# Kernel tuning notes

Measured on AMD Instinct MI355X. Metric: run time of the kernel, lower is better.

The kernel has to match this reference:

```python
import jax, jax.numpy as jnp
import numpy as np

B, P, K, HE, HF = 256, 128, 512, 1024, 512
D = K + HE + 2 * HF  # 2560, MLP input dim
HID = 64


def setup_inputs() -> dict:
    key = jax.random.key(0)
    ks = jax.random.split(key, 6)
    query = jax.random.normal(ks[0], (B, 1, HE), dtype=jnp.float32)
    keys = jax.random.normal(ks[1], (B, P, K), dtype=jnp.float32)
    frameLSTM_h = jax.random.normal(ks[2], (B, 1, 2 * HF), dtype=jnp.float32)
    mask = jax.random.randint(ks[3], (B, P), 0, 2, dtype=jnp.int32)
    mask = mask.at[:, 0].set(1)  # guarantee at least one unmasked player per row
    W1 = jax.random.normal(ks[4], (D, HID), dtype=jnp.float32) / np.float32(np.sqrt(D))
    W2 = jax.random.normal(ks[5], (HID, 1), dtype=jnp.float32) / np.float32(np.sqrt(HID))
    return dict(query=query, keys=keys, frameLSTM_h=frameLSTM_h, mask=mask, W1=W1, W2=W2)


def reference(query, keys, frameLSTM_h, mask, W1, W2):
    # Faithful to: cat([keys, query.repeat, frame.repeat]) @ W1 -> ReLU -> @ W2.
    # The pre-activation is linear, so splitting W1 by row-blocks is exactly the
    # same math without materializing the repeated/concatenated (B,P,D) tensor.
    W1k = W1[:K]            # (K, 64)
    W1q = W1[K:K + HE]      # (HE, 64)
    W1f = W1[K + HE:]       # (2*HF, 64)
    h = jax.nn.relu(
        jnp.einsum('bpk,kh->bph', keys, W1k)
        + jnp.einsum('boe,eh->boh', query, W1q)        # broadcasts over P
        + jnp.einsum('bof,fh->boh', frameLSTM_h, W1f)  # broadcasts over P
    )  # (B, P, 64)
    raw_scores = jnp.einsum('bph,ho->bp', h, W2)  # (B, P)
    raw_scores = jnp.where(mask == 0, -jnp.inf, raw_scores)
    weights = jax.nn.softmax(raw_scores, axis=1)  # (B, P)
    context = jnp.einsum('bp,bpk->bk', weights, keys)[:, None, :]  # (B, 1, K)
    embeddings = jnp.concatenate([context, frameLSTM_h], axis=2)   # (B, 1, K+2*HF)
    return embeddings, weights
```

## Files before the change

### kernel.cpp

```cpp
#include <hip/hip_runtime.h>
#include <hip/hip_bf16.h>
#include <cstdint>
#include <math.h>


typedef __bf16 bf16;
typedef __attribute__((ext_vector_type(8))) __bf16 bf16x8;
typedef __attribute__((ext_vector_type(4))) __bf16 bf16x4;
typedef __attribute__((ext_vector_type(4))) float f32x4;

#define NB 256
#define NP 128
#define NK 512
#define SKLD 520
#define SK_BYTES (NP * SKLD * 2)
#define SMEM_BYTES (SK_BYTES + 128*4 + 128*4 + 256*4 + 64*4)

__global__ __launch_bounds__(256) void prep_kernel(
    const float* __restrict__ W1, bf16* __restrict__ w1kt,
    bf16* __restrict__ w1qft)
{
    const int blk = blockIdx.x;
    const int t = threadIdx.x;
    __shared__ float s[32][65];
    if (blk < 16) {
        const int k0 = blk * 32;
#pragma unroll
        for (int i = 0; i < 8; i++) {
            const int idx = t + 256 * i;
            const int k = idx >> 6, h = idx & 63;
            s[k][h] = W1[(size_t)(k0 + k) * 64 + h];
        }
        __syncthreads();
#pragma unroll
        for (int i = 0; i < 8; i++) {
            const int idx = t + 256 * i;
            const int h = idx >> 5, kk = idx & 31;
            w1kt[(size_t)h * 512 + k0 + kk] = (bf16)s[kk][h];
        }
    } else {
        const int j = blk - 16;
        const int d0 = j * 32;
#pragma unroll
        for (int i = 0; i < 8; i++) {
            const int idx = t + 256 * i;
            const int r = idx >> 6, h = idx & 63;
            s[r][h] = W1[(size_t)(512 + d0 + r) * 64 + h];
        }
        __syncthreads();
#pragma unroll
        for (int i = 0; i < 8; i++) {
            const int idx = t + 256 * i;
            const int h = idx >> 5, rr = idx & 31;
            w1qft[(size_t)h * 2048 + d0 + rr] = (bf16)s[rr][h];
        }
    }
}

__global__ __launch_bounds__(256) void attn_kernel(
    const float* __restrict__ keys, const float* __restrict__ query,
    const float* __restrict__ frame, const int* __restrict__ mask,
    const float* __restrict__ W2, const bf16* __restrict__ w1kt,
    const bf16* __restrict__ w1qft, float* __restrict__ out)
{
    extern __shared__ char smem[];
    bf16* sk      = (bf16*)smem;
    float* scores = (float*)(smem + SK_BYTES);
    float* wts    = scores + 128;
    float* pp     = wts + 128;
    float* w2l    = pp + 256;

    const int b = blockIdx.x;
    const int t = threadIdx.x;
    const int w = t >> 6;
    const int lane = t & 63;
    const int m = lane & 15;
    const int q = lane >> 4;

    if (t < 64) w2l[t] = W2[t];

    {
        const float* qf = (w < 2 ? query : frame) + (size_t)b * 1024 + (w & 1) * 512;
        const bf16* wb = w1qft + (size_t)m * 2048 + w * 512 + q * 8;
        f32x4 pacc[4];
#pragma unroll
        for (int nt = 0; nt < 4; nt++) pacc[nt] = (f32x4){0.f, 0.f, 0.f, 0.f};

        float4 qa = *(const float4*)(qf + q * 8);
        float4 qb = *(const float4*)(qf + q * 8 + 4);
        bf16x8 Bp[4];
#pragma unroll
        for (int nt = 0; nt < 4; nt++) Bp[nt] = *(const bf16x8*)(wb + nt * 32768);

#pragma unroll
        for (int kk = 0; kk < 16; kk++) {
            bf16x8 Af;
            Af[0] = (bf16)qa.x; Af[1] = (bf16)qa.y; Af[2] = (bf16)qa.z; Af[3] = (bf16)qa.w;
            Af[4] = (bf16)qb.x; Af[5] = (bf16)qb.y; Af[6] = (bf16)qb.z; Af[7] = (bf16)qb.w;
            bf16x8 Bc[4];
#pragma unroll
            for (int nt = 0; nt < 4; nt++) Bc[nt] = Bp[nt];
            if (kk < 15) {
                qa = *(const float4*)(qf + (kk + 1) * 32 + q * 8);
                qb = *(const float4*)(qf + (kk + 1) * 32 + q * 8 + 4);
#pragma unroll
                for (int nt = 0; nt < 4; nt++)
                    Bp[nt] = *(const bf16x8*)(wb + nt * 32768 + (kk + 1) * 32);
            }
#pragma unroll
            for (int nt = 0; nt < 4; nt++)
                pacc[nt] = __builtin_amdgcn_mfma_f32_16x16x32_bf16(Af, Bc[nt], pacc[nt], 0, 0, 0);
        }
        if (q == 0) {
#pragma unroll
            for (int nt = 0; nt < 4; nt++)
                pp[w * 64 + nt * 16 + m] = pacc[nt][0];
        }
    }

    const float* kb = keys + (size_t)b * (NP * NK);
    {
        const int rowadd = t >> 7;
        const int c0 = (t & 127) * 4;
        float4 kv[2][16];
#pragma unroll
        for (int ii = 0; ii < 16; ii++)
            kv[0][ii] = *(const float4*)(kb + (size_t)ii * 1024 + t * 4);
#pragma unroll
        for (int jj = 0; jj < 4; jj++) {
            const int cur = jj & 1;
            if (jj < 3) {
#pragma unroll
                for (int ii = 0; ii < 16; ii++)
                    kv[cur ^ 1][ii] =
                        *(const float4*)(kb + (size_t)((jj + 1) * 16 + ii) * 1024 + t * 4);
            }
#pragma unroll
            for (int ii = 0; ii < 16; ii++) {
                const float4 v = kv[cur][ii];
                bf16x4 bv;
                bv[0] = (bf16)v.x; bv[1] = (bf16)v.y;
                bv[2] = (bf16)v.z; bv[3] = (bf16)v.w;
                *(bf16x4*)(sk + (size_t)(2 * (jj * 16 + ii) + rowadd) * SKLD + c0) = bv;
            }
        }
    }
    __syncthreads();

    const int pw = w * 32;
    const bf16* bbase = w1kt + (size_t)m * 512 + q * 8;

    bf16x8 Bv[2][16];
#pragma unroll
    for (int kk = 0; kk < 16; kk++)
        Bv[0][kk] = *(const bf16x8*)(bbase + kk * 32);

    float pr[2][4] = {{0.f,0.f,0.f,0.f},{0.f,0.f,0.f,0.f}};

#pragma unroll
    for (int nt = 0; nt < 4; nt++) {
        const int cur = nt & 1;
        if (nt < 3) {
#pragma unroll
            for (int kk = 0; kk < 16; kk++)
                Bv[cur ^ 1][kk] = *(const bf16x8*)(bbase + (nt + 1) * 8192 + kk * 32);
        }
        f32x4 acc0 = (f32x4){0.f,0.f,0.f,0.f};
        f32x4 acc1 = (f32x4){0.f,0.f,0.f,0.f};
#pragma unroll
        for (int kk = 0; kk < 16; kk++) {
            const int k0 = kk * 32 + q * 8;
            const bf16x8 A0 = *(const bf16x8*)(sk + (pw + m) * SKLD + k0);
            const bf16x8 A1 = *(const bf16x8*)(sk + (pw + 16 + m) * SKLD + k0);
            acc0 = __builtin_amdgcn_mfma_f32_16x16x32_bf16(A0, Bv[cur][kk], acc0, 0, 0, 0);
            acc1 = __builtin_amdgcn_mfma_f32_16x16x32_bf16(A1, Bv[cur][kk], acc1, 0, 0, 0);
        }
        const int h = nt * 16 + m;
        const float pv = pp[h] + pp[64 + h] + pp[128 + h] + pp[192 + h];
        const float wv = w2l[h];
#pragma unroll
        for (int r = 0; r < 4; r++) {
            pr[0][r] += fmaxf(acc0[r] + pv, 0.f) * wv;
            pr[1][r] += fmaxf(acc1[r] + pv, 0.f) * wv;
        }
    }

#pragma unroll
    for (int off = 1; off < 16; off <<= 1) {
#pragma unroll
        for (int mt = 0; mt < 2; mt++)
#pragma unroll
            for (int r = 0; r < 4; r++)
                pr[mt][r] += __shfl_xor(pr[mt][r], off);
    }
    if (m == 0) {
#pragma unroll
        for (int mt = 0; mt < 2; mt++) {
            const int pbase = pw + mt * 16 + q * 4;
#pragma unroll
            for (int r = 0; r < 4; r++) scores[pbase + r] = pr[mt][r];
        }
    }
    __syncthreads();

    if (w == 0) {
        const int pa = lane, pb = lane + 64;
        float s0 = (mask[b * 128 + pa] == 0) ? -INFINITY : scores[pa];
        float s1 = (mask[b * 128 + pb] == 0) ? -INFINITY : scores[pb];
        float mx = fmaxf(s0, s1);
#pragma unroll
        for (int off = 32; off; off >>= 1) mx = fmaxf(mx, __shfl_xor(mx, off));
        float e0 = __expf(s0 - mx), e1 = __expf(s1 - mx);
        float sum = e0 + e1;
#pragma unroll
        for (int off = 32; off; off >>= 1) sum += __shfl_xor(sum, off);
        const float inv = 1.0f / sum;
        e0 *= inv; e1 *= inv;
        wts[pa] = e0; wts[pb] = e1;
        float* wout = out + (size_t)NB * 1536;
        wout[b * 128 + pa] = e0;
        wout[b * 128 + pb] = e1;
    }
    __syncthreads();

    {
        float a0 = 0.f, a1 = 0.f;
        const int c = 2 * t;
#pragma unroll 8
        for (int p = 0; p < 128; p++) {
            const float wv = wts[p];
            const uint32_t uv = *(const uint32_t*)(sk + p * SKLD + c);
            a0 += wv * __uint_as_float(uv << 16);
            a1 += wv * __uint_as_float(uv & 0xffff0000u);
        }
        out[(size_t)b * 1536 + c] = a0;
        out[(size_t)b * 1536 + c + 1] = a1;
    }
    {
        const float4 fv = *(const float4*)(frame + (size_t)b * 1024 + t * 4);
        *(float4*)(out + (size_t)b * 1536 + 512 + t * 4) = fv;
    }
}

extern "C" void kernel_launch(void* const* d_in, const int* in_sizes, int n_in,
                              void* d_out, int out_size, void* d_ws, size_t ws_size,
                              hipStream_t stream) {
    const float* query = (const float*)d_in[0];
    const float* keys  = (const float*)d_in[1];
    const float* frame = (const float*)d_in[2];
    const int*   mask  = (const int*)d_in[3];
    const float* W1    = (const float*)d_in[4];
    const float* W2    = (const float*)d_in[5];
    float* out = (float*)d_out;

    bf16* w1kt  = (bf16*)d_ws;
    bf16* w1qft = (bf16*)((char*)d_ws + (64 << 10));

    hipFuncSetAttribute((const void*)attn_kernel,
                        hipFuncAttributeMaxDynamicSharedMemorySize, SMEM_BYTES);

    prep_kernel<<<80, 256, 0, stream>>>(W1, w1kt, w1qft);
    attn_kernel<<<256, 256, SMEM_BYTES, stream>>>(keys, query, frame, mask, W2,
                                                  w1kt, w1qft, out);
}
```

Baseline: 124.6 us.

## Move query/frame projection to prep kernel and fuse keys load with MFMA

The per-batch query/frame projection moves out of the attention kernel into the prep kernel, which now computes it in fp32 for 4 batches per block. The attention kernel uses 512 threads, and each wave streams its 16 key rows straight from global memory into bf16 MFMA operands while also writing them to shared memory. This removes the separate staging pass and the extra sync before the score GEMM. The context reduction now gives each thread one column. The trade-off is a serial fp32 dot-product loop in the prep kernel that may take longer, and more threads per block.

New measurement: 154.7 us. +24.2%, slower.

```diff
diff --git a/kernel.cpp b/kernel.cpp
--- a/kernel.cpp
+++ b/kernel.cpp
@@ -6,7 +6,6 @@
 
 typedef __bf16 bf16;
 typedef __attribute__((ext_vector_type(8))) __bf16 bf16x8;
-typedef __attribute__((ext_vector_type(4))) __bf16 bf16x4;
 typedef __attribute__((ext_vector_type(4))) float f32x4;
 
 #define NB 256
@@ -14,16 +13,17 @@
 #define NK 512
 #define SKLD 520
 #define SK_BYTES (NP * SKLD * 2)
-#define SMEM_BYTES (SK_BYTES + 128*4 + 128*4 + 256*4 + 64*4)
+#define SMEM_BYTES (SK_BYTES + 128 * 4 + 128 * 4)
 
 __global__ __launch_bounds__(256) void prep_kernel(
-    const float* __restrict__ W1, bf16* __restrict__ w1kt,
-    bf16* __restrict__ w1qft)
+    const float* __restrict__ W1, const float* __restrict__ query,
+    const float* __restrict__ frame, bf16* __restrict__ w1kt,
+    float* __restrict__ proj)
 {
     const int blk = blockIdx.x;
     const int t = threadIdx.x;
-    __shared__ float s[32][65];
     if (blk < 16) {
+        __shared__ float s[32][65];
         const int k0 = blk * 32;
 #pragma unroll
         for (int i = 0; i < 8; i++) {
@@ -39,36 +39,43 @@
             w1kt[(size_t)h * 512 + k0 + kk] = (bf16)s[kk][h];
         }
     } else {
-        const int j = blk - 16;
-        const int d0 = j * 32;
-#pragma unroll
-        for (int i = 0; i < 8; i++) {
-            const int idx = t + 256 * i;
-            const int r = idx >> 6, h = idx & 63;
-            s[r][h] = W1[(size_t)(512 + d0 + r) * 64 + h];
-        }
+        __shared__ float red[4][4][64];
+        const int b0 = (blk - 16) * 4;
+        const int c = t >> 6;
+        const int h = t & 63;
+        const float* q0 = (c < 2) ? (query + c * 512) : (frame + (c - 2) * 512);
+        const float* w1r = W1 + (size_t)(512 + c * 512) * 64 + h;
+        float a0[4] = {0.f, 0.f, 0.f, 0.f};
+        float a1[4] = {0.f, 0.f, 0.f, 0.f};
+#pragma unroll 4
+        for (int d = 0; d < 512; d += 2) {
+            const float w0  = w1r[(size_t)d * 64];
+            const float w1v = w1r[(size_t)(d + 1) * 64];
+#pragma unroll
+            for (int j = 0; j < 4; j++) {
+                a0[j] += q0[(size_t)(b0 + j) * 1024 + d] * w0;
+                a1[j] += q0[(size_t)(b0 + j) * 1024 + d + 1] * w1v;
+            }
+        }
+#pragma unroll
+        for (int j = 0; j < 4; j++) red[c][j][h] = a0[j] + a1[j];
         __syncthreads();
-#pragma unroll
-        for (int i = 0; i < 8; i++) {
-            const int idx = t + 256 * i;
-            const int h = idx >> 5, rr = idx & 31;
-            w1qft[(size_t)h * 2048 + d0 + rr] = (bf16)s[rr][h];
-        }
+        const int j2 = t >> 6;
+        proj[(size_t)(b0 + j2) * 64 + h] =
+            red[0][j2][h] + red[1][j2][h] + red[2][j2][h] + red[3][j2][h];
     }
 }
 
-__global__ __launch_bounds__(256) void attn_kernel(
-    const float* __restrict__ keys, const float* __restrict__ query,
-    const float* __restrict__ frame, const int* __restrict__ mask,
-    const float* __restrict__ W2, const bf16* __restrict__ w1kt,
-    const bf16* __restrict__ w1qft, float* __restrict__ out)
+__global__ __launch_bounds__(512) void attn_kernel(
+    const float* __restrict__ keys, const float* __restrict__ frame,
+    const int* __restrict__ mask, const float* __restrict__ W2,
+    const bf16* __restrict__ w1kt, const float* __restrict__ proj,
+    float* __restrict__ out)
 {
     extern __shared__ char smem[];
     bf16* sk      = (bf16*)smem;
     float* scores = (float*)(smem + SK_BYTES);
     float* wts    = scores + 128;
-    float* pp     = wts + 128;
-    float* w2l    = pp + 256;
 
     const int b = blockIdx.x;
     const int t = threadIdx.x;
@@ -76,135 +83,72 @@
     const int lane = t & 63;
     const int m = lane & 15;
     const int q = lane >> 4;
-
-    if (t < 64) w2l[t] = W2[t];
-
-    {
-        const float* qf = (w < 2 ? query : frame) + (size_t)b * 1024 + (w & 1) * 512;
-        const bf16* wb = w1qft + (size_t)m * 2048 + w * 512 + q * 8;
-        f32x4 pacc[4];
-#pragma unroll
-        for (int nt = 0; nt < 4; nt++) pacc[nt] = (f32x4){0.f, 0.f, 0.f, 0.f};
-
-        float4 qa = *(const float4*)(qf + q * 8);
-        float4 qb = *(const float4*)(qf + q * 8 + 4);
-        bf16x8 Bp[4];
-#pragma unroll
-        for (int nt = 0; nt < 4; nt++) Bp[nt] = *(const bf16x8*)(wb + nt * 32768);
-
-#pragma unroll
-        for (int kk = 0; kk < 16; kk++) {
-            bf16x8 Af;
-            Af[0] = (bf16)qa.x; Af[1] = (bf16)qa.y; Af[2] = (bf16)qa.z; Af[3] = (bf16)qa.w;
-            Af[4] = (bf16)qb.x; Af[5] = (bf16)qb.y; Af[6] = (bf16)qb.z; Af[7] = (bf16)qb.w;
-            bf16x8 Bc[4];
-#pragma unroll
-            for (int nt = 0; nt < 4; nt++) Bc[nt] = Bp[nt];
-            if (kk < 15) {
-                qa = *(const float4*)(qf + (kk + 1) * 32 + q * 8);
-                qb = *(const float4*)(qf + (kk + 1) * 32 + q * 8 + 4);
-#pragma unroll
-                for (int nt = 0; nt < 4; nt++)
-                    Bp[nt] = *(const bf16x8*)(wb + nt * 32768 + (kk + 1) * 32);
-            }
+    const int p0 = w * 16;
+
+    float pv[4], wv[4];
+#pragma unroll
+    for (int nt = 0; nt < 4; nt++) {
+        pv[nt] = proj[b * 64 + nt * 16 + m];
+        wv[nt] = W2[nt * 16 + m];
+    }
+
+    const float* arow = keys + (size_t)b * (NP * NK) + (size_t)(p0 + m) * NK + q * 8;
+    const bf16* bb = w1kt + m * 512 + q * 8;
+    bf16* swr = sk + (size_t)(p0 + m) * SKLD + q * 8;
+
+    f32x4 acc[4];
+#pragma unroll
+    for (int nt = 0; nt < 4; nt++) acc[nt] = (f32x4){0.f, 0.f, 0.f, 0.f};
+
+    float4 Aa[2], Ab[2];
+    bf16x8 Bp[2][4];
+    Aa[0] = *(const float4*)(arow);
+    Ab[0] = *(const float4*)(arow + 4);
+#pragma unroll
+    for (int nt = 0; nt < 4; nt++) Bp[0][nt] = *(const bf16x8*)(bb + nt * 8192);
+
+#pragma unroll
+    for (int kk = 0; kk < 16; kk++) {
+        const int cur = kk & 1;
+        if (kk < 15) {
+            Aa[cur ^ 1] = *(const float4*)(arow + (kk + 1) * 32);
+            Ab[cur ^ 1] = *(const float4*)(arow + (kk + 1) * 32 + 4);
 #pragma unroll
             for (int nt = 0; nt < 4; nt++)
-                pacc[nt] = __builtin_amdgcn_mfma_f32_16x16x32_bf16(Af, Bc[nt], pacc[nt], 0, 0, 0);
-        }
-        if (q == 0) {
-#pragma unroll
-            for (int nt = 0; nt < 4; nt++)
-                pp[w * 64 + nt * 16 + m] = pacc[nt][0];
-        }
-    }
-
-    const float* kb = keys + (size_t)b * (NP * NK);
-    {
-        const int rowadd = t >> 7;
-        const int c0 = (t & 127) * 4;
-        float4 kv[2][16];
-#pragma unroll
-        for (int ii = 0; ii < 16; ii++)
-            kv[0][ii] = *(const float4*)(kb + (size_t)ii * 1024 + t * 4);
-#pragma unroll
-        for (int jj = 0; jj < 4; jj++) {
-            const int cur = jj & 1;
-            if (jj < 3) {
-#pragma unroll
-                for (int ii = 0; ii < 16; ii++)
-                    kv[cur ^ 1][ii] =
-                        *(const float4*)(kb + (size_t)((jj + 1) * 16 + ii) * 1024 + t * 4);
-            }
-#pragma unroll
-            for (int ii = 0; ii < 16; ii++) {
-                const float4 v = kv[cur][ii];
-                bf16x4 bv;
-                bv[0] = (bf16)v.x; bv[1] = (bf16)v.y;
-                bv[2] = (bf16)v.z; bv[3] = (bf16)v.w;
-                *(bf16x4*)(sk + (size_t)(2 * (jj * 16 + ii) + rowadd) * SKLD + c0) = bv;
-            }
-        }
+                Bp[cur ^ 1][nt] = *(const bf16x8*)(bb + nt * 8192 + (kk + 1) * 32);
+        }
+        bf16x8 Af;
+        Af[0] = (bf16)Aa[cur].x; Af[1] = (bf16)Aa[cur].y;
+        Af[2] = (bf16)Aa[cur].z; Af[3] = (bf16)Aa[cur].w;
+        Af[4] = (bf16)Ab[cur].x; Af[5] = (bf16)Ab[cur].y;
+        Af[6] = (bf16)Ab[cur].z; Af[7] = (bf16)Ab[cur].w;
+        *(bf16x8*)(swr + kk * 32) = Af;
+#pragma unroll
+        for (int nt = 0; nt < 4; nt++)
+            acc[nt] = __builtin_amdgcn_mfma_f32_16x16x32_bf16(Af, Bp[cur][nt], acc[nt], 0, 0, 0);
+    }
+
+    float pr[4] = {0.f, 0.f, 0.f, 0.f};
+#pragma unroll
+    for (int nt = 0; nt < 4; nt++)
+#pragma unroll
+        for (int r = 0; r < 4; r++)
+            pr[r] += fmaxf(acc[nt][r] + pv[nt], 0.f) * wv[nt];
+
+#pragma unroll
+    for (int off = 1; off < 16; off <<= 1)
+#pragma unroll
+        for (int r = 0; r < 4; r++)
+            pr[r] += __shfl_xor(pr[r], off);
+
+    if (m == 0) {
+#pragma unroll
+        for (int r = 0; r < 4; r++) scores[p0 + q * 4 + r] = pr[r];
     }
     __syncthreads();
 
-    const int pw = w * 32;
-    const bf16* bbase = w1kt + (size_t)m * 512 + q * 8;
-
-    bf16x8 Bv[2][16];
-#pragma unroll
-    for (int kk = 0; kk < 16; kk++)
-        Bv[0][kk] = *(const bf16x8*)(bbase + kk * 32);
-
-    float pr[2][4] = {{0.f,0.f,0.f,0.f},{0.f,0.f,0.f,0.f}};
-
-#pragma unroll
-    for (int nt = 0; nt < 4; nt++) {
-        const int cur = nt & 1;
-        if (nt < 3) {
-#pragma unroll
-            for (int kk = 0; kk < 16; kk++)
-                Bv[cur ^ 1][kk] = *(const bf16x8*)(bbase + (nt + 1) * 8192 + kk * 32);
-        }
-        f32x4 acc0 = (f32x4){0.f,0.f,0.f,0.f};
-        f32x4 acc1 = (f32x4){0.f,0.f,0.f,0.f};
-#pragma unroll
-        for (int kk = 0; kk < 16; kk++) {
-            const int k0 = kk * 32 + q * 8;
-            const bf16x8 A0 = *(const bf16x8*)(sk + (pw + m) * SKLD + k0);
-            const bf16x8 A1 = *(const bf16x8*)(sk + (pw + 16 + m) * SKLD + k0);
-            acc0 = __builtin_amdgcn_mfma_f32_16x16x32_bf16(A0, Bv[cur][kk], acc0, 0, 0, 0);
-            acc1 = __builtin_amdgcn_mfma_f32_16x16x32_bf16(A1, Bv[cur][kk], acc1, 0, 0, 0);
-        }
-        const int h = nt * 16 + m;
-        const float pv = pp[h] + pp[64 + h] + pp[128 + h] + pp[192 + h];
-        const float wv = w2l[h];
-#pragma unroll
-        for (int r = 0; r < 4; r++) {
-            pr[0][r] += fmaxf(acc0[r] + pv, 0.f) * wv;
-            pr[1][r] += fmaxf(acc1[r] + pv, 0.f) * wv;
-        }
-    }
-
-#pragma unroll
-    for (int off = 1; off < 16; off <<= 1) {
-#pragma unroll
-        for (int mt = 0; mt < 2; mt++)
-#pragma unroll
-            for (int r = 0; r < 4; r++)
-                pr[mt][r] += __shfl_xor(pr[mt][r], off);
-    }
-    if (m == 0) {
-#pragma unroll
-        for (int mt = 0; mt < 2; mt++) {
-            const int pbase = pw + mt * 16 + q * 4;
-#pragma unroll
-            for (int r = 0; r < 4; r++) scores[pbase + r] = pr[mt][r];
-        }
-    }
-    __syncthreads();
-
-    if (w == 0) {
-        const int pa = lane, pb = lane + 64;
+    if (t < 64) {
+        const int pa = t, pb = t + 64;
         float s0 = (mask[b * 128 + pa] == 0) ? -INFINITY : scores[pa];
         float s1 = (mask[b * 128 + pb] == 0) ? -INFINITY : scores[pb];
         float mx = fmaxf(s0, s1);
@@ -224,19 +168,17 @@
     __syncthreads();
 
     {
-        float a0 = 0.f, a1 = 0.f;
-        const int c = 2 * t;
+        float c0 = 0.f, c1 = 0.f;
 #pragma unroll 8
-        for (int p = 0; p < 128; p++) {
-            const float wv = wts[p];
-            const uint32_t uv = *(const uint32_t*)(sk + p * SKLD + c);
-            a0 += wv * __uint_as_float(uv << 16);
-            a1 += wv * __uint_as_float(uv & 0xffff0000u);
-        }
-        out[(size_t)b * 1536 + c] = a0;
-        out[(size_t)b * 1536 + c + 1] = a1;
-    }
-    {
+        for (int p = 0; p < 128; p += 2) {
+            const uint32_t u0 = (uint32_t)*(const uint16_t*)(sk + (size_t)p * SKLD + t);
+            const uint32_t u1 = (uint32_t)*(const uint16_t*)(sk + (size_t)(p + 1) * SKLD + t);
+            c0 += wts[p] * __uint_as_float(u0 << 16);
+            c1 += wts[p + 1] * __uint_as_float(u1 << 16);
+        }
+        out[(size_t)b * 1536 + t] = c0 + c1;
+    }
+    if (t < 256) {
         const float4 fv = *(const float4*)(frame + (size_t)b * 1024 + t * 4);
         *(float4*)(out + (size_t)b * 1536 + 512 + t * 4) = fv;
     }
@@ -254,12 +196,12 @@
     float* out = (float*)d_out;
 
     bf16* w1kt  = (bf16*)d_ws;
-    bf16* w1qft = (bf16*)((char*)d_ws + (64 << 10));
+    float* proj = (float*)((char*)d_ws + (64 << 10));
 
     hipFuncSetAttribute((const void*)attn_kernel,
                         hipFuncAttributeMaxDynamicSharedMemorySize, SMEM_BYTES);
 
-    prep_kernel<<<80, 256, 0, stream>>>(W1, w1kt, w1qft);
-    attn_kernel<<<256, 256, SMEM_BYTES, stream>>>(keys, query, frame, mask, W2,
-                                                  w1kt, w1qft, out);
+    prep_kernel<<<80, 256, 0, stream>>>(W1, query, frame, w1kt, proj);
+    attn_kernel<<<256, 512, SMEM_BYTES, stream>>>(keys, frame, mask, W2,
+                                                  w1kt, proj, out);
 }
```
